# Kernel optimization log

Hardware: AMD Instinct MI355X
Metric: run time of the kernel (lower is better)

## Reference

```python
import jax, jax.numpy as jnp
import numpy as np

B, T, KD, QD, AD, VD, W = 16, 4096, 1024, 1024, 512, 1024, 8


def moving_sum(x, back, forward):
    # x: [B, T] -> windowed sum over [t-back, t+forward], matches F.conv1d with ones filter
    xp = jnp.pad(x, ((0, 0), (back, forward)))[:, None, :]
    filt = jnp.ones((1, 1, back + forward + 1), x.dtype)
    y = jax.lax.conv_general_dilated(xp, filt, (1,), 'VALID')
    return y[:, 0, :]


def setup_inputs() -> dict:
    key = jax.random.key(0)
    ks = jax.random.split(key, 16)
    inp = {
        'key': jax.random.normal(ks[0], (B, T, KD), jnp.float32),
        'value': jax.random.normal(ks[1], (B, T, VD), jnp.float32),
        'query': jax.random.normal(ks[2], (B, 1, QD), jnp.float32),
        'noise': jax.random.normal(ks[3], (B, T), jnp.float32),
        'Wk_mono': jax.random.normal(ks[4], (KD, AD), jnp.float32) * (KD ** -0.5),
        'b_mono': jnp.zeros((AD,), jnp.float32),
        'Wq_mono': jax.random.normal(ks[5], (QD, AD), jnp.float32) * (QD ** -0.5),
        'Wk_chunk': jax.random.normal(ks[6], (KD, AD), jnp.float32) * (KD ** -0.5),
        'b_chunk': jnp.zeros((AD,), jnp.float32),
        'Wq_chunk': jax.random.normal(ks[7], (QD, AD), jnp.float32) * (QD ** -0.5),
        'r_mono': jnp.array([-4.0], jnp.float32),
        'r_chunk': jnp.array([-4.0], jnp.float32),
    }
    # weight-normalized v vectors: g = sqrt(1/attn_dim), w = g * v/||v||
    g = (1.0 / AD) ** 0.5
    vm = jax.random.normal(ks[8], (AD,), jnp.float32)
    vc = jax.random.normal(ks[9], (AD,), jnp.float32)
    inp['v_mono'] = g * vm / jnp.linalg.norm(vm)
    inp['v_chunk'] = g * vc / jnp.linalg.norm(vc)
    return inp


def _forward(key, value, query, noise, Wk_mono, b_mono, Wq_mono, v_mono, r_mono,
             Wk_chunk, b_chunk, Wq_chunk, v_chunk, r_chunk):
    bs, kmax = key.shape[0], key.shape[1]
    # aw_prev default: one-hot at position 0
    aw_prev = jnp.zeros((bs, kmax), key.dtype).at[:, 0].set(1.0)

    # monotonic energy: [B, T]
    qm = jnp.einsum('bqd,da->bqa', query, Wq_mono)  # [B,1,A], broadcasts over T
    e_mono = jnp.einsum('bta,a->bt', jnp.tanh(key @ Wk_mono + b_mono + qm), v_mono) + r_mono

    # parallel mode: sigmoid with additive gaussian noise
    p_choose = jax.nn.sigmoid(e_mono + noise)
    # safe_cumprod with the original's exclusive_cumsum (prepends ONES, drops last)
    log1mp = jnp.log(jnp.clip(1.0 - p_choose, 1e-10, 1.0))
    shifted = jnp.concatenate([jnp.ones((bs, 1), key.dtype), log1mp[:, :-1]], axis=1)
    cumprod_1mp = jnp.exp(jnp.cumsum(shifted, axis=1))
    aw = p_choose * cumprod_1mp * jnp.cumsum(
        aw_prev / jnp.clip(cumprod_1mp, 1e-10, 1.0), axis=1)

    # chunk energy
    qc = jnp.einsum('bqd,da->bqa', query, Wq_chunk)
    e_chunk = jnp.einsum('bta,a->bt', jnp.tanh(key @ Wk_chunk + b_chunk + qc), v_chunk) + r_chunk

    # efficient chunkwise attention
    u = e_chunk - jnp.max(e_chunk, axis=1, keepdims=True)
    softmax_exp = jnp.maximum(jnp.exp(u), 1e-5)
    denom = moving_sum(softmax_exp, back=W - 1, forward=0)
    beta = softmax_exp * moving_sum(aw / denom, back=0, forward=W - 1)

    cv = jnp.einsum('bt,btd->bd', beta, value)[:, None, :]  # [B,1,VD]
    return cv, aw[..., None]


def reference(key, value, query, noise, Wk_mono, b_mono, Wq_mono, v_mono, r_mono,
              Wk_chunk, b_chunk, Wq_chunk, v_chunk, r_chunk):
    return _forward(key, value, query, noise, Wk_mono, b_mono, Wq_mono, v_mono, r_mono,
                    Wk_chunk, b_chunk, Wq_chunk, v_chunk, r_chunk)
```

## Files before the change

### kernel.cpp

```cpp
#include <hip/hip_runtime.h>
#include <hip/hip_bf16.h>
#include <math.h>

#define B_   16
#define T_   4096
#define KD_  1024
#define AD_  512
#define VD_  1024

typedef float f32x4 __attribute__((ext_vector_type(4)));
typedef short s16x8 __attribute__((ext_vector_type(8)));

static __device__ __forceinline__ short f2bf(float f) {
    __hip_bfloat16 h = __float2bfloat16(f);
    return __builtin_bit_cast(short, h);
}

static __device__ __forceinline__ float fast_tanh(float x) {
    x = fminf(fmaxf(x, -15.f), 15.f);
    float e = __expf(2.f * x);
    return (e - 1.f) / (e + 1.f);
}

static __device__ __forceinline__ void gload16(const void* g, void* l) {
    __builtin_amdgcn_global_load_lds(
        (const __attribute__((address_space(1))) void*)(g),
        (__attribute__((address_space(3))) void*)(l), 16, 0, 0);
}


__global__ __launch_bounds__(256) void qproj_kernel(
    const float* __restrict__ query,
    const float* __restrict__ Wq_mono, const float* __restrict__ b_mono,
    const float* __restrict__ Wq_chunk, const float* __restrict__ b_chunk,
    float* __restrict__ qb) {
    __shared__ float red[4][64];
    int b = blockIdx.x;
    int mat = blockIdx.y;
    int ac = blockIdx.z;
    const float* Wq = mat ? Wq_chunk : Wq_mono;
    const float* bb = mat ? b_chunk : b_mono;
    int al = threadIdx.x & 63;
    int dg = threadIdx.x >> 6;
    int a = ac * 64 + al;
    const float* q = query + b * KD_ + dg * 256;
    const float* wp = Wq + (size_t)(dg * 256) * AD_ + a;
    float s = 0.f;
#pragma unroll 4
    for (int d = 0; d < 256; ++d)
        s += q[d] * wp[(size_t)d * AD_];
    red[dg][al] = s;
    __syncthreads();
    if (dg == 0) {
        float t = red[0][al] + red[1][al] + red[2][al] + red[3][al];
        qb[(mat * B_ + b) * AD_ + a] = t + bb[a];
    }
}

__global__ __launch_bounds__(256) void wtrans_kernel(
    const float* __restrict__ Wk_mono, const float* __restrict__ Wk_chunk,
    short* __restrict__ WkTB) {
    __shared__ float tile[32][33];
    int n0 = blockIdx.x * 32;
    int k0 = blockIdx.y * 32;
    int tx = threadIdx.x;
    int ty = threadIdx.y;
    int tid = ty * 32 + tx;
    const float* src;
    int nloc;
    if (n0 < 512) { src = Wk_mono;  nloc = n0; }
    else          { src = Wk_chunk; nloc = n0 - 512; }
#pragma unroll
    for (int i = 0; i < 4; ++i) {
        int k = ty + i * 8;
        tile[k][tx] = src[(size_t)(k0 + k) * AD_ + nloc + tx];
    }
    __syncthreads();
    if (tid < 128) {
        int r = tid >> 2;
        int sub = tid & 3;
        s16x8 h;
#pragma unroll
        for (int j = 0; j < 8; ++j)
            h[j] = f2bf(tile[sub * 8 + j][r]);
        int n = n0 + r;
        int nblk = n >> 7;
        int rloc = n & 127;
        int kt = k0 >> 5;
        int c = (rloc << 2) | (sub ^ ((rloc >> 1) & 3));
        *reinterpret_cast<s16x8*>(WkTB + (((size_t)(nblk * 32 + kt) * 512 + c) << 3)) = h;
    }
}

__global__ __launch_bounds__(256) void gemm_e_kernel(
    const float* __restrict__ key,
    const short* __restrict__ WkTB,
    const float* __restrict__ qb,
    const float* __restrict__ v_mono, const float* __restrict__ v_chunk,
    float* __restrict__ e_ws ) {
    __shared__ short As[2][128 * 32];
    __shared__ short Bs[2][128 * 32];
    int tid = threadIdx.x;
    int bid = blockIdx.x;
    int swz = (bid & 7) * 512 + (bid >> 3);
    int mt = swz >> 3;
    int nt = swz & 7;
    int mBase = mt * 128;
    int nBase = nt * 128;
    int lane = tid & 63;
    int wid = tid >> 6;
    int wr = wid >> 1, wc = wid & 1;
    int col16 = lane & 15, g4 = lane >> 4;

    int c0 = wid * 128 + lane;
    int c1 = c0 + 64;
    const short* pB0 = WkTB + (((size_t)nt * 32) * 512 + c0) * 8;
    const short* pB1 = WkTB + (((size_t)nt * 32) * 512 + c1) * 8;
    int sOff0 = (wid * 128 + 0) * 8;
    int sOff1 = (wid * 128 + 64) * 8;

    int arow = tid >> 1;
    int ad0 = (tid & 1) * 2;
    const float* pA = key + (size_t)(mBase + arow) * KD_ + ad0 * 8;
    int aswz = (arow >> 1) & 3;
    int aslot0 = (arow * 4 + (ad0 ^ aswz)) * 8;
    int aslot1 = (arow * 4 + ((ad0 + 1) ^ aswz)) * 8;

    int aoff[4], boff[4];
#pragma unroll
    for (int m = 0; m < 4; ++m) {
        int row = wr * 64 + m * 16 + col16;
        aoff[m] = (row * 4 + (g4 ^ ((row >> 1) & 3))) * 8;
    }
#pragma unroll
    for (int n = 0; n < 4; ++n) {
        int row = wc * 64 + n * 16 + col16;
        boff[n] = (row * 4 + (g4 ^ ((row >> 1) & 3))) * 8;
    }

    f32x4 zero4 = {0.f, 0.f, 0.f, 0.f};
    f32x4 acc[4][4];
#pragma unroll
    for (int m = 0; m < 4; ++m)
#pragma unroll
        for (int n = 0; n < 4; ++n) acc[m][n] = zero4;

    gload16(pB0, &Bs[0][sOff0]);
    gload16(pB1, &Bs[0][sOff1]);
    pB0 += 4096; pB1 += 4096;
    {
        f32x4 q0 = *reinterpret_cast<const f32x4*>(pA);
        f32x4 q1 = *reinterpret_cast<const f32x4*>(pA + 4);
        f32x4 q2 = *reinterpret_cast<const f32x4*>(pA + 8);
        f32x4 q3 = *reinterpret_cast<const f32x4*>(pA + 12);
        s16x8 h0, h1;
        h0[0]=f2bf(q0[0]); h0[1]=f2bf(q0[1]); h0[2]=f2bf(q0[2]); h0[3]=f2bf(q0[3]);
        h0[4]=f2bf(q1[0]); h0[5]=f2bf(q1[1]); h0[6]=f2bf(q1[2]); h0[7]=f2bf(q1[3]);
        h1[0]=f2bf(q2[0]); h1[1]=f2bf(q2[1]); h1[2]=f2bf(q2[2]); h1[3]=f2bf(q2[3]);
        h1[4]=f2bf(q3[0]); h1[5]=f2bf(q3[1]); h1[6]=f2bf(q3[2]); h1[7]=f2bf(q3[3]);
        *reinterpret_cast<s16x8*>(&As[0][aslot0]) = h0;
        *reinterpret_cast<s16x8*>(&As[0][aslot1]) = h1;
    }
    const float* pAn = pA + 32;
    __syncthreads();

    int cur = 0;
    for (int kt = 0; kt < 31; ++kt) {
        int nxt = cur ^ 1;
        gload16(pB0, &Bs[nxt][sOff0]);
        gload16(pB1, &Bs[nxt][sOff1]);
        pB0 += 4096; pB1 += 4096;
        f32x4 q0 = *reinterpret_cast<const f32x4*>(pAn);
        f32x4 q1 = *reinterpret_cast<const f32x4*>(pAn + 4);
        f32x4 q2 = *reinterpret_cast<const f32x4*>(pAn + 8);
        f32x4 q3 = *reinterpret_cast<const f32x4*>(pAn + 12);
        pAn += 32;
        s16x8 af[4], bfr[4];
#pragma unroll
        for (int m = 0; m < 4; ++m)
            af[m] = *reinterpret_cast<const s16x8*>(&As[cur][aoff[m]]);
#pragma unroll
        for (int n = 0; n < 4; ++n)
            bfr[n] = *reinterpret_cast<const s16x8*>(&Bs[cur][boff[n]]);
#pragma unroll
        for (int m = 0; m < 4; ++m)
#pragma unroll
            for (int n = 0; n < 4; ++n)
                acc[m][n] = __builtin_amdgcn_mfma_f32_16x16x32_bf16(af[m], bfr[n], acc[m][n], 0, 0, 0);
        s16x8 h0, h1;
        h0[0]=f2bf(q0[0]); h0[1]=f2bf(q0[1]); h0[2]=f2bf(q0[2]); h0[3]=f2bf(q0[3]);
        h0[4]=f2bf(q1[0]); h0[5]=f2bf(q1[1]); h0[6]=f2bf(q1[2]); h0[7]=f2bf(q1[3]);
        h1[0]=f2bf(q2[0]); h1[1]=f2bf(q2[1]); h1[2]=f2bf(q2[2]); h1[3]=f2bf(q2[3]);
        h1[4]=f2bf(q3[0]); h1[5]=f2bf(q3[1]); h1[6]=f2bf(q3[2]); h1[7]=f2bf(q3[3]);
        *reinterpret_cast<s16x8*>(&As[nxt][aslot0]) = h0;
        *reinterpret_cast<s16x8*>(&As[nxt][aslot1]) = h1;
        __syncthreads();
        cur = nxt;
    }
    {
        s16x8 af[4], bfr[4];
#pragma unroll
        for (int m = 0; m < 4; ++m)
            af[m] = *reinterpret_cast<const s16x8*>(&As[cur][aoff[m]]);
#pragma unroll
        for (int n = 0; n < 4; ++n)
            bfr[n] = *reinterpret_cast<const s16x8*>(&Bs[cur][boff[n]]);
#pragma unroll
        for (int m = 0; m < 4; ++m)
#pragma unroll
            for (int n = 0; n < 4; ++n)
                acc[m][n] = __builtin_amdgcn_mfma_f32_16x16x32_bf16(af[m], bfr[n], acc[m][n], 0, 0, 0);
    }

    int bIdx = mBase >> 12;
    int matrix = nBase >> 9;
    int aBase = (nBase & 511) + wc * 64 + col16;
    const float* qbRow = qb + (matrix * B_ + bIdx) * AD_;
    const float* vv = matrix ? v_chunk : v_mono;
    float* eArr = e_ws + matrix * (B_ * T_);
    float qcol[4], vcol[4];
#pragma unroll
    for (int n = 0; n < 4; ++n) {
        int a = aBase + n * 16;
        qcol[n] = qbRow[a];
        vcol[n] = vv[a];
    }
#pragma unroll
    for (int m = 0; m < 4; ++m) {
        float s0 = 0.f, s1 = 0.f, s2 = 0.f, s3 = 0.f;
#pragma unroll
        for (int n = 0; n < 4; ++n) {
            s0 += fast_tanh(acc[m][n][0] + qcol[n]) * vcol[n];
            s1 += fast_tanh(acc[m][n][1] + qcol[n]) * vcol[n];
            s2 += fast_tanh(acc[m][n][2] + qcol[n]) * vcol[n];
            s3 += fast_tanh(acc[m][n][3] + qcol[n]) * vcol[n];
        }
#pragma unroll
        for (int mask = 1; mask < 16; mask <<= 1) {
            s0 += __shfl_xor(s0, mask, 64);
            s1 += __shfl_xor(s1, mask, 64);
            s2 += __shfl_xor(s2, mask, 64);
            s3 += __shfl_xor(s3, mask, 64);
        }
        if (col16 == 0) {
            int rowB = mBase + wr * 64 + m * 16 + g4 * 4;
            atomicAdd(&eArr[rowB + 0], s0);
            atomicAdd(&eArr[rowB + 1], s1);
            atomicAdd(&eArr[rowB + 2], s2);
            atomicAdd(&eArr[rowB + 3], s3);
        }
    }
}

__global__ __launch_bounds__(256) void scan_kernel(
    const float* __restrict__ e_ws,
    const float* __restrict__ noise,
    const float* __restrict__ r_mono, const float* __restrict__ r_chunk,
    float* __restrict__ aw_out, float* __restrict__ beta_out) {
    __shared__ float s_aw[T_];
    __shared__ float s_sexp[T_];
    __shared__ float s_ad[T_];
    __shared__ float s_w[4];
    int b = blockIdx.x;
    int tid = threadIdx.x;
    int lane = tid & 63;
    int wid4 = tid >> 6;
    int t0 = tid * 16;
    const float* em = e_ws + b * T_;
    const float* ec = e_ws + B_ * T_ + b * T_;
    const float* nz = noise + b * T_;
    float rm = r_mono[0], rc = r_chunk[0];

    float pv[16], lp[16];
    float run = 0.f;
#pragma unroll
    for (int j = 0; j < 16; ++j) {
        float x = em[t0 + j] + rm + nz[t0 + j];
        float p = 1.f / (1.f + expf(-x));
        pv[j] = p;
        float om = fminf(fmaxf(1.f - p, 1e-10f), 1.f);
        lp[j] = run;
        run += logf(om);
    }
    float x = run;
#pragma unroll
    for (int off = 1; off < 64; off <<= 1) {
        float y = __shfl_up(x, off, 64);
        if (lane >= off) x += y;
    }
    if (lane == 63) s_w[wid4] = x;
    __syncthreads();
    float wbase = 0.f;
#pragma unroll
    for (int i = 0; i < 3; ++i) if (i < wid4) wbase += s_w[i];
    float base = 1.f + (wbase + x - run);
#pragma unroll
    for (int j = 0; j < 16; ++j) {
        float aw = pv[j] * expf(base + lp[j]);
        s_aw[t0 + j] = aw;
        aw_out[b * T_ + t0 + j] = aw;
    }
    float evs[16];
    float lmax = -INFINITY;
#pragma unroll
    for (int j = 0; j < 16; ++j) {
        float v = ec[t0 + j] + rc;
        evs[j] = v;
        lmax = fmaxf(lmax, v);
    }
#pragma unroll
    for (int off = 1; off < 64; off <<= 1)
        lmax = fmaxf(lmax, __shfl_xor(lmax, off, 64));
    __syncthreads();
    if (lane == 0) s_w[wid4] = lmax;
    __syncthreads();
    float mx = fmaxf(fmaxf(s_w[0], s_w[1]), fmaxf(s_w[2], s_w[3]));
#pragma unroll
    for (int j = 0; j < 16; ++j)
        s_sexp[t0 + j] = fmaxf(expf(evs[j] - mx), 1e-5f);
    __syncthreads();
#pragma unroll
    for (int j = 0; j < 16; ++j) {
        int t = t0 + j;
        int lo = t - 7; if (lo < 0) lo = 0;
        float d = 0.f;
        for (int i = lo; i <= t; ++i) d += s_sexp[i];
        s_ad[t] = s_aw[t] / d;
    }
    __syncthreads();
#pragma unroll
    for (int j = 0; j < 16; ++j) {
        int t = t0 + j;
        int hi = t + 7; if (hi > T_ - 1) hi = T_ - 1;
        float m2 = 0.f;
        for (int i = t; i <= hi; ++i) m2 += s_ad[i];
        beta_out[b * T_ + t] = s_sexp[t] * m2;
    }
}

__global__ __launch_bounds__(256) void cv_kernel(
    const float* __restrict__ value,
    const float* __restrict__ beta,
    float* __restrict__ cv) {
    __shared__ float s_beta[128];
    int b = blockIdx.x;
    int tc = blockIdx.y;
    int tid = threadIdx.x;
    int t0 = tc * 128;
    if (tid < 128) s_beta[tid] = beta[b * T_ + t0 + tid];
    __syncthreads();
    int d0 = tid * 4;
    f32x4 acc = {0.f, 0.f, 0.f, 0.f};
    const float* vp = value + (size_t)(b * T_ + t0) * VD_ + d0;
#pragma unroll 4
    for (int i = 0; i < 128; ++i) {
        f32x4 v = *reinterpret_cast<const f32x4*>(vp + (size_t)i * VD_);
        float bt = s_beta[i];
        acc[0] += bt * v[0];
        acc[1] += bt * v[1];
        acc[2] += bt * v[2];
        acc[3] += bt * v[3];
    }
    atomicAdd(&cv[b * VD_ + d0 + 0], acc[0]);
    atomicAdd(&cv[b * VD_ + d0 + 1], acc[1]);
    atomicAdd(&cv[b * VD_ + d0 + 2], acc[2]);
    atomicAdd(&cv[b * VD_ + d0 + 3], acc[3]);
}

extern "C" void kernel_launch(void* const* d_in, const int* in_sizes, int n_in,
                              void* d_out, int out_size, void* d_ws, size_t ws_size,
                              hipStream_t stream) {
    const float* key      = (const float*)d_in[0];
    const float* value    = (const float*)d_in[1];
    const float* query    = (const float*)d_in[2];
    const float* noise    = (const float*)d_in[3];
    const float* Wk_mono  = (const float*)d_in[4];
    const float* b_mono   = (const float*)d_in[5];
    const float* Wq_mono  = (const float*)d_in[6];
    const float* Wk_chunk = (const float*)d_in[7];
    const float* b_chunk  = (const float*)d_in[8];
    const float* Wq_chunk = (const float*)d_in[9];
    const float* r_mono   = (const float*)d_in[10];
    const float* r_chunk  = (const float*)d_in[11];
    const float* v_mono   = (const float*)d_in[12];
    const float* v_chunk  = (const float*)d_in[13];
    float* out = (float*)d_out;

    char* ws = (char*)d_ws;
    size_t off = 0;
    float* e_ws = (float*)(ws + off); off += 2 * B_ * T_ * sizeof(float);
    float* qb   = (float*)(ws + off); off += 2 * B_ * AD_ * sizeof(float);
    short* WkTB = (short*)(ws + off); off += (size_t)KD_ * KD_ * 2;
    float* beta = (float*)(ws + off); off += B_ * T_ * sizeof(float);

    hipMemsetAsync(e_ws, 0, 2 * B_ * T_ * sizeof(float), stream);
    hipMemsetAsync(out, 0, B_ * VD_ * sizeof(float), stream);

    qproj_kernel<<<dim3(16, 2, 8), 256, 0, stream>>>(query, Wq_mono, b_mono, Wq_chunk, b_chunk, qb);
    wtrans_kernel<<<dim3(32, 32), dim3(32, 8), 0, stream>>>(Wk_mono, Wk_chunk, WkTB);
    gemm_e_kernel<<<4096, 256, 0, stream>>>(key, WkTB, qb, v_mono, v_chunk, e_ws);
    scan_kernel<<<16, 256, 0, stream>>>(e_ws, noise, r_mono, r_chunk, out + B_ * VD_, beta);
    cv_kernel<<<dim3(16, 32), 256, 0, stream>>>(value, beta, out);
}
```

Before: 392.6 us.

## Pre-convert key to blocked bf16 and stream both GEMM operands directly to LDS

A new kernel converts the fp32 key tensor to bf16 and writes it in the same swizzled tiled layout the GEMM reads from LDS. The GEMM can then load both A and B tiles with direct global-to-LDS loads, dropping the per-iteration fp32 register loads, bf16 conversion and LDS stores. The GEMM tile also grows to 256x128 with 512 threads, which raises reuse of each B tile. The cost is an extra full pass over key: a 256 MB read and a 128 MB write, plus a large extra workspace buffer.

```diff
diff --git a/kernel.cpp b/kernel.cpp
--- a/kernel.cpp
+++ b/kernel.cpp
@@ -28,6 +28,28 @@
         (__attribute__((address_space(3))) void*)(l), 16, 0, 0);
 }
 
+
+__global__ __launch_bounds__(256) void cvt_key_blk_kernel(
+    const float* __restrict__ key, short* __restrict__ keyB) {
+    const size_t nchunk = (size_t)B_ * T_ * KD_ / 8;
+    size_t stride = (size_t)gridDim.x * 256;
+    for (size_t g = (size_t)blockIdx.x * 256 + threadIdx.x; g < nchunk; g += stride) {
+        const float* p = key + g * 8;
+        f32x4 f0 = *reinterpret_cast<const f32x4*>(p);
+        f32x4 f1 = *reinterpret_cast<const f32x4*>(p + 4);
+        s16x8 h;
+        h[0] = f2bf(f0[0]); h[1] = f2bf(f0[1]); h[2] = f2bf(f0[2]); h[3] = f2bf(f0[3]);
+        h[4] = f2bf(f1[0]); h[5] = f2bf(f1[1]); h[6] = f2bf(f1[2]); h[7] = f2bf(f1[3]);
+        size_t m = g >> 7;
+        int kc = (int)(g & 127);
+        size_t mt = m >> 8;
+        int r = (int)(m & 255);
+        int kt = kc >> 2;
+        int sub = kc & 3;
+        int c = (r << 2) | (sub ^ ((r >> 1) & 3));
+        *reinterpret_cast<s16x8*>(keyB + (((mt * 32 + kt) * 1024 + c) << 3)) = h;
+    }
+}
 
 __global__ __launch_bounds__(256) void qproj_kernel(
     const float* __restrict__ query,
@@ -92,39 +114,35 @@
     }
 }
 
-__global__ __launch_bounds__(256) void gemm_e_kernel(
-    const float* __restrict__ key,
+__global__ __launch_bounds__(512) void gemm_e_kernel(
+    const short* __restrict__ keyB,
     const short* __restrict__ WkTB,
     const float* __restrict__ qb,
     const float* __restrict__ v_mono, const float* __restrict__ v_chunk,
     float* __restrict__ e_ws ) {
-    __shared__ short As[2][128 * 32];
+    __shared__ short As[2][256 * 32];
     __shared__ short Bs[2][128 * 32];
     int tid = threadIdx.x;
     int bid = blockIdx.x;
-    int swz = (bid & 7) * 512 + (bid >> 3);
+    int swz = (bid & 7) * 256 + (bid >> 3);
     int mt = swz >> 3;
     int nt = swz & 7;
-    int mBase = mt * 128;
+    int mBase = mt * 256;
     int nBase = nt * 128;
     int lane = tid & 63;
     int wid = tid >> 6;
     int wr = wid >> 1, wc = wid & 1;
     int col16 = lane & 15, g4 = lane >> 4;
 
-    int c0 = wid * 128 + lane;
-    int c1 = c0 + 64;
-    const short* pB0 = WkTB + (((size_t)nt * 32) * 512 + c0) * 8;
-    const short* pB1 = WkTB + (((size_t)nt * 32) * 512 + c1) * 8;
-    int sOff0 = (wid * 128 + 0) * 8;
-    int sOff1 = (wid * 128 + 64) * 8;
-
-    int arow = tid >> 1;
-    int ad0 = (tid & 1) * 2;
-    const float* pA = key + (size_t)(mBase + arow) * KD_ + ad0 * 8;
-    int aswz = (arow >> 1) & 3;
-    int aslot0 = (arow * 4 + (ad0 ^ aswz)) * 8;
-    int aslot1 = (arow * 4 + ((ad0 + 1) ^ aswz)) * 8;
+    int cA0 = wid * 64 + lane;
+    int cA1 = cA0 + 512;
+    int cB  = wid * 64 + lane;
+    const short* pA0 = keyB + ((size_t)mt * 32 * 1024 + cA0) * 8;
+    const short* pA1 = keyB + ((size_t)mt * 32 * 1024 + cA1) * 8;
+    const short* pB  = WkTB + ((size_t)nt * 32 * 512 + cB) * 8;
+    int sA0 = (wid * 64) * 8;
+    int sA1 = (512 + wid * 64) * 8;
+    int sB  = (wid * 64) * 8;
 
     int aoff[4], boff[4];
 #pragma unroll
@@ -145,36 +163,19 @@
 #pragma unroll
         for (int n = 0; n < 4; ++n) acc[m][n] = zero4;
 
-    gload16(pB0, &Bs[0][sOff0]);
-    gload16(pB1, &Bs[0][sOff1]);
-    pB0 += 4096; pB1 += 4096;
-    {
-        f32x4 q0 = *reinterpret_cast<const f32x4*>(pA);
-        f32x4 q1 = *reinterpret_cast<const f32x4*>(pA + 4);
-        f32x4 q2 = *reinterpret_cast<const f32x4*>(pA + 8);
-        f32x4 q3 = *reinterpret_cast<const f32x4*>(pA + 12);
-        s16x8 h0, h1;
-        h0[0]=f2bf(q0[0]); h0[1]=f2bf(q0[1]); h0[2]=f2bf(q0[2]); h0[3]=f2bf(q0[3]);
-        h0[4]=f2bf(q1[0]); h0[5]=f2bf(q1[1]); h0[6]=f2bf(q1[2]); h0[7]=f2bf(q1[3]);
-        h1[0]=f2bf(q2[0]); h1[1]=f2bf(q2[1]); h1[2]=f2bf(q2[2]); h1[3]=f2bf(q2[3]);
-        h1[4]=f2bf(q3[0]); h1[5]=f2bf(q3[1]); h1[6]=f2bf(q3[2]); h1[7]=f2bf(q3[3]);
-        *reinterpret_cast<s16x8*>(&As[0][aslot0]) = h0;
-        *reinterpret_cast<s16x8*>(&As[0][aslot1]) = h1;
-    }
-    const float* pAn = pA + 32;
+    gload16(pA0, &As[0][sA0]);
+    gload16(pA1, &As[0][sA1]);
+    gload16(pB,  &Bs[0][sB]);
+    pA0 += 8192; pA1 += 8192; pB += 4096;
     __syncthreads();
 
     int cur = 0;
     for (int kt = 0; kt < 31; ++kt) {
         int nxt = cur ^ 1;
-        gload16(pB0, &Bs[nxt][sOff0]);
-        gload16(pB1, &Bs[nxt][sOff1]);
-        pB0 += 4096; pB1 += 4096;
-        f32x4 q0 = *reinterpret_cast<const f32x4*>(pAn);
-        f32x4 q1 = *reinterpret_cast<const f32x4*>(pAn + 4);
-        f32x4 q2 = *reinterpret_cast<const f32x4*>(pAn + 8);
-        f32x4 q3 = *reinterpret_cast<const f32x4*>(pAn + 12);
-        pAn += 32;
+        gload16(pA0, &As[nxt][sA0]);
+        gload16(pA1, &As[nxt][sA1]);
+        gload16(pB,  &Bs[nxt][sB]);
+        pA0 += 8192; pA1 += 8192; pB += 4096;
         s16x8 af[4], bfr[4];
 #pragma unroll
         for (int m = 0; m < 4; ++m)
@@ -187,13 +188,6 @@
 #pragma unroll
             for (int n = 0; n < 4; ++n)
                 acc[m][n] = __builtin_amdgcn_mfma_f32_16x16x32_bf16(af[m], bfr[n], acc[m][n], 0, 0, 0);
-        s16x8 h0, h1;
-        h0[0]=f2bf(q0[0]); h0[1]=f2bf(q0[1]); h0[2]=f2bf(q0[2]); h0[3]=f2bf(q0[3]);
-        h0[4]=f2bf(q1[0]); h0[5]=f2bf(q1[1]); h0[6]=f2bf(q1[2]); h0[7]=f2bf(q1[3]);
-        h1[0]=f2bf(q2[0]); h1[1]=f2bf(q2[1]); h1[2]=f2bf(q2[2]); h1[3]=f2bf(q2[3]);
-        h1[4]=f2bf(q3[0]); h1[5]=f2bf(q3[1]); h1[6]=f2bf(q3[2]); h1[7]=f2bf(q3[3]);
-        *reinterpret_cast<s16x8*>(&As[nxt][aslot0]) = h0;
-        *reinterpret_cast<s16x8*>(&As[nxt][aslot1]) = h1;
         __syncthreads();
         cur = nxt;
     }
@@ -392,13 +386,15 @@
     float* qb   = (float*)(ws + off); off += 2 * B_ * AD_ * sizeof(float);
     short* WkTB = (short*)(ws + off); off += (size_t)KD_ * KD_ * 2;
     float* beta = (float*)(ws + off); off += B_ * T_ * sizeof(float);
+    short* keyB = (short*)(ws + off);
 
     hipMemsetAsync(e_ws, 0, 2 * B_ * T_ * sizeof(float), stream);
     hipMemsetAsync(out, 0, B_ * VD_ * sizeof(float), stream);
 
     qproj_kernel<<<dim3(16, 2, 8), 256, 0, stream>>>(query, Wq_mono, b_mono, Wq_chunk, b_chunk, qb);
     wtrans_kernel<<<dim3(32, 32), dim3(32, 8), 0, stream>>>(Wk_mono, Wk_chunk, WkTB);
-    gemm_e_kernel<<<4096, 256, 0, stream>>>(key, WkTB, qb, v_mono, v_chunk, e_ws);
+    cvt_key_blk_kernel<<<4096, 256, 0, stream>>>(key, keyB);
+    gemm_e_kernel<<<2048, 512, 0, stream>>>(keyB, WkTB, qb, v_mono, v_chunk, e_ws);
     scan_kernel<<<16, 256, 0, stream>>>(e_ws, noise, r_mono, r_chunk, out + B_ * VD_, beta);
     cv_kernel<<<dim3(16, 32), 256, 0, stream>>>(value, beta, out);
 }
```

After: 370.4 us. -5.6%, faster.

## Stage fp32 key tiles via async global-to-LDS loads, convert to bf16 at fragment read

Applied to the files above, without the earlier changes.

The A operand (fp32 key) was previously loaded into registers, converted to bf16 and stored to LDS by each thread. It now goes straight from global memory into an fp32 LDS buffer with direct global-to-LDS loads and an XOR swizzle, and is converted to bf16 when the MFMA fragments are read. This is meant to remove register round-trips and VALU conversion from the load path and overlap the key fetch with compute. In exchange LDS use for A doubles (32KB per stage), more LDS read bandwidth is needed, and conversion work is repeated per wave, since each wave converts the fragments it reads.

```diff
diff --git a/kernel.cpp b/kernel.cpp
--- a/kernel.cpp
+++ b/kernel.cpp
@@ -98,7 +98,7 @@
     const float* __restrict__ qb,
     const float* __restrict__ v_mono, const float* __restrict__ v_chunk,
     float* __restrict__ e_ws ) {
-    __shared__ short As[2][128 * 32];
+    __shared__ float Asf[2][128 * 32];
     __shared__ short Bs[2][128 * 32];
     int tid = threadIdx.x;
     int bid = blockIdx.x;
@@ -112,25 +112,34 @@
     int wr = wid >> 1, wc = wid & 1;
     int col16 = lane & 15, g4 = lane >> 4;
 
-    int c0 = wid * 128 + lane;
-    int c1 = c0 + 64;
-    const short* pB0 = WkTB + (((size_t)nt * 32) * 512 + c0) * 8;
-    const short* pB1 = WkTB + (((size_t)nt * 32) * 512 + c1) * 8;
-    int sOff0 = (wid * 128 + 0) * 8;
-    int sOff1 = (wid * 128 + 64) * 8;
-
-    int arow = tid >> 1;
-    int ad0 = (tid & 1) * 2;
-    const float* pA = key + (size_t)(mBase + arow) * KD_ + ad0 * 8;
-    int aswz = (arow >> 1) & 3;
-    int aslot0 = (arow * 4 + (ad0 ^ aswz)) * 8;
-    int aslot1 = (arow * 4 + ((ad0 + 1) ^ aswz)) * 8;
-
-    int aoff[4], boff[4];
+    const float* pA[4];
+    int sAf[4];
+#pragma unroll
+    for (int i = 0; i < 4; ++i) {
+        int c = i * 256 + tid;
+        int r = c >> 3;
+        int ss = c & 7;
+        int sd = ss ^ (r & 7);
+        pA[i] = key + (size_t)(mBase + r) * KD_ + sd * 4;
+        sAf[i] = (i * 256 + wid * 64) * 16;
+    }
+#pragma unroll
+    for (int i = 0; i < 4; ++i) sAf[i] = (i * 256 + wid * 64) * 4;
+
+    int cB0 = wid * 128 + lane;
+    int cB1 = cB0 + 64;
+    const short* pB0 = WkTB + (((size_t)nt * 32) * 512 + cB0) * 8;
+    const short* pB1 = WkTB + (((size_t)nt * 32) * 512 + cB1) * 8;
+    int sB0 = (wid * 128 + 0) * 8;
+    int sB1 = (wid * 128 + 64) * 8;
+
+    int aoff0[4], aoff1[4];
+    int boff[4];
 #pragma unroll
     for (int m = 0; m < 4; ++m) {
         int row = wr * 64 + m * 16 + col16;
-        aoff[m] = (row * 4 + (g4 ^ ((row >> 1) & 3))) * 8;
+        aoff0[m] = (row * 8 + ((g4 * 2)     ^ (row & 7))) * 4;
+        aoff1[m] = (row * 8 + ((g4 * 2 + 1) ^ (row & 7))) * 4;
     }
 #pragma unroll
     for (int n = 0; n < 4; ++n) {
@@ -145,40 +154,35 @@
 #pragma unroll
         for (int n = 0; n < 4; ++n) acc[m][n] = zero4;
 
-    gload16(pB0, &Bs[0][sOff0]);
-    gload16(pB1, &Bs[0][sOff1]);
+#pragma unroll
+    for (int i = 0; i < 4; ++i) gload16(pA[i], &Asf[0][sAf[i]]);
+    gload16(pB0, &Bs[0][sB0]);
+    gload16(pB1, &Bs[0][sB1]);
+#pragma unroll
+    for (int i = 0; i < 4; ++i) pA[i] += 32;
     pB0 += 4096; pB1 += 4096;
-    {
-        f32x4 q0 = *reinterpret_cast<const f32x4*>(pA);
-        f32x4 q1 = *reinterpret_cast<const f32x4*>(pA + 4);
-        f32x4 q2 = *reinterpret_cast<const f32x4*>(pA + 8);
-        f32x4 q3 = *reinterpret_cast<const f32x4*>(pA + 12);
-        s16x8 h0, h1;
-        h0[0]=f2bf(q0[0]); h0[1]=f2bf(q0[1]); h0[2]=f2bf(q0[2]); h0[3]=f2bf(q0[3]);
-        h0[4]=f2bf(q1[0]); h0[5]=f2bf(q1[1]); h0[6]=f2bf(q1[2]); h0[7]=f2bf(q1[3]);
-        h1[0]=f2bf(q2[0]); h1[1]=f2bf(q2[1]); h1[2]=f2bf(q2[2]); h1[3]=f2bf(q2[3]);
-        h1[4]=f2bf(q3[0]); h1[5]=f2bf(q3[1]); h1[6]=f2bf(q3[2]); h1[7]=f2bf(q3[3]);
-        *reinterpret_cast<s16x8*>(&As[0][aslot0]) = h0;
-        *reinterpret_cast<s16x8*>(&As[0][aslot1]) = h1;
-    }
-    const float* pAn = pA + 32;
     __syncthreads();
 
     int cur = 0;
     for (int kt = 0; kt < 31; ++kt) {
         int nxt = cur ^ 1;
-        gload16(pB0, &Bs[nxt][sOff0]);
-        gload16(pB1, &Bs[nxt][sOff1]);
+#pragma unroll
+        for (int i = 0; i < 4; ++i) gload16(pA[i], &Asf[nxt][sAf[i]]);
+        gload16(pB0, &Bs[nxt][sB0]);
+        gload16(pB1, &Bs[nxt][sB1]);
+#pragma unroll
+        for (int i = 0; i < 4; ++i) pA[i] += 32;
         pB0 += 4096; pB1 += 4096;
-        f32x4 q0 = *reinterpret_cast<const f32x4*>(pAn);
-        f32x4 q1 = *reinterpret_cast<const f32x4*>(pAn + 4);
-        f32x4 q2 = *reinterpret_cast<const f32x4*>(pAn + 8);
-        f32x4 q3 = *reinterpret_cast<const f32x4*>(pAn + 12);
-        pAn += 32;
         s16x8 af[4], bfr[4];
 #pragma unroll
-        for (int m = 0; m < 4; ++m)
-            af[m] = *reinterpret_cast<const s16x8*>(&As[cur][aoff[m]]);
+        for (int m = 0; m < 4; ++m) {
+            f32x4 a0 = *reinterpret_cast<const f32x4*>(&Asf[cur][aoff0[m]]);
+            f32x4 a1 = *reinterpret_cast<const f32x4*>(&Asf[cur][aoff1[m]]);
+            s16x8 h;
+            h[0] = f2bf(a0[0]); h[1] = f2bf(a0[1]); h[2] = f2bf(a0[2]); h[3] = f2bf(a0[3]);
+            h[4] = f2bf(a1[0]); h[5] = f2bf(a1[1]); h[6] = f2bf(a1[2]); h[7] = f2bf(a1[3]);
+            af[m] = h;
+        }
 #pragma unroll
         for (int n = 0; n < 4; ++n)
             bfr[n] = *reinterpret_cast<const s16x8*>(&Bs[cur][boff[n]]);
@@ -187,21 +191,20 @@
 #pragma unroll
             for (int n = 0; n < 4; ++n)
                 acc[m][n] = __builtin_amdgcn_mfma_f32_16x16x32_bf16(af[m], bfr[n], acc[m][n], 0, 0, 0);
-        s16x8 h0, h1;
-        h0[0]=f2bf(q0[0]); h0[1]=f2bf(q0[1]); h0[2]=f2bf(q0[2]); h0[3]=f2bf(q0[3]);
-        h0[4]=f2bf(q1[0]); h0[5]=f2bf(q1[1]); h0[6]=f2bf(q1[2]); h0[7]=f2bf(q1[3]);
-        h1[0]=f2bf(q2[0]); h1[1]=f2bf(q2[1]); h1[2]=f2bf(q2[2]); h1[3]=f2bf(q2[3]);
-        h1[4]=f2bf(q3[0]); h1[5]=f2bf(q3[1]); h1[6]=f2bf(q3[2]); h1[7]=f2bf(q3[3]);
-        *reinterpret_cast<s16x8*>(&As[nxt][aslot0]) = h0;
-        *reinterpret_cast<s16x8*>(&As[nxt][aslot1]) = h1;
         __syncthreads();
         cur = nxt;
     }
     {
         s16x8 af[4], bfr[4];
 #pragma unroll
-        for (int m = 0; m < 4; ++m)
-            af[m] = *reinterpret_cast<const s16x8*>(&As[cur][aoff[m]]);
+        for (int m = 0; m < 4; ++m) {
+            f32x4 a0 = *reinterpret_cast<const f32x4*>(&Asf[cur][aoff0[m]]);
+            f32x4 a1 = *reinterpret_cast<const f32x4*>(&Asf[cur][aoff1[m]]);
+            s16x8 h;
+            h[0] = f2bf(a0[0]); h[1] = f2bf(a0[1]); h[2] = f2bf(a0[2]); h[3] = f2bf(a0[3]);
+            h[4] = f2bf(a1[0]); h[5] = f2bf(a1[1]); h[6] = f2bf(a1[2]); h[7] = f2bf(a1[3]);
+            af[m] = h;
+        }
 #pragma unroll
         for (int n = 0; n < 4; ++n)
             bfr[n] = *reinterpret_cast<const s16x8*>(&Bs[cur][boff[n]]);
```

New measurement: 534.5 us. 36.1% more time.
